# Kernel tuning notes

Measured on AMD Instinct MI355X. Metric: run time of the kernel, lower is better.

The kernel has to match this reference:

```python
import jax, jax.numpy as jnp
import numpy as np

GAMMA = 0.99
GAE_LAMBDA = 0.95
DONE_PROB = 0.01  # sparse episode terminations, typical for long-horizon trading envs


def setup_inputs() -> dict:
    key = jax.random.key(0)
    k1, k2, k3 = jax.random.split(key, 3)
    T, N = 2048, 4096  # rollout_len, num_envs
    rewards = jax.random.normal(k1, (T, N), dtype=jnp.float32)
    values = jax.random.normal(k2, (T, N), dtype=jnp.float32)
    dones = (jax.random.uniform(k3, (T, N)) < DONE_PROB).astype(jnp.float32)
    return {"rewards": rewards, "values": values, "dones": dones}


def reference(rewards, values, dones):
    # rewards/values/dones: [T, N]
    T, N = rewards.shape
    # bootstrap: beyond the last step, next_value = 0 and next_done = 1
    next_value = jnp.concatenate([values[1:], jnp.zeros((1, N), values.dtype)], axis=0)
    next_done = jnp.concatenate([dones[1:], jnp.ones((1, N), dones.dtype)], axis=0)
    nonterminal = 1.0 - next_done                      # [T, N]
    delta = rewards + GAMMA * next_value * nonterminal - values  # [T, N]

    def step(last_adv, xs):
        d, nt = xs                                     # each [N]
        adv = d + GAMMA * GAE_LAMBDA * nt * last_adv
        return adv, adv

    init = jnp.zeros((N,), rewards.dtype)
    _, advantages = jax.lax.scan(step, init, (delta, nonterminal), reverse=True)
    returns = advantages + values
    return advantages, returns
```

## Files before the change

### kernel.cpp

```cpp
#include <hip/hip_runtime.h>


#define T_LEN    2048
#define N_ENV    4096
#define NV4      (N_ENV / 4)
#define N_CHUNKS 128
#define CHUNK_L  (T_LEN / N_CHUNKS)

static constexpr float GAMMA = 0.99f;
static constexpr float GL    = 0.99f * 0.95f;

__global__ __launch_bounds__(256) void gae_phase1(
    const float4* __restrict__ rewards,
    const float4* __restrict__ values,
    const float4* __restrict__ dones,
    float4* __restrict__ Aout,
    float4* __restrict__ Pout)
{
    const int idx = blockIdx.x * blockDim.x + threadIdx.x;
    const int n4 = idx & (NV4 - 1);
    const int c  = idx >> 10;
    const int t_hi = c * CHUNK_L + (CHUNK_L - 1);

    float4 v_next, d_next;
    if (c == N_CHUNKS - 1) {
        v_next = make_float4(0.f, 0.f, 0.f, 0.f);
        d_next = make_float4(1.f, 1.f, 1.f, 1.f);
    } else {
        v_next = values[(t_hi + 1) * NV4 + n4];
        d_next = dones [(t_hi + 1) * NV4 + n4];
    }

    float4 A = make_float4(1.f, 1.f, 1.f, 1.f);
    float4 P = make_float4(0.f, 0.f, 0.f, 0.f);

    #pragma unroll
    for (int i = 0; i < CHUNK_L; ++i) {
        const int t = t_hi - i;
        const float4 r = rewards[t * NV4 + n4];
        const float4 v = values [t * NV4 + n4];
        const float4 d = dones  [t * NV4 + n4];
        #define STEP(X) { \
            const float nt    = 1.0f - d_next.X; \
            const float delta = fmaf(GAMMA * v_next.X, nt, r.X) - v.X; \
            const float cc    = GL * nt; \
            P.X = fmaf(cc, P.X, delta); \
            A.X = cc * A.X; \
            v_next.X = v.X; d_next.X = d.X; }
        STEP(x) STEP(y) STEP(z) STEP(w)
        #undef STEP
    }
    Aout[idx] = A;
    Pout[idx] = P;
}

__global__ __launch_bounds__(256) void gae_phase23(
    const float4* __restrict__ rewards,
    const float4* __restrict__ values,
    const float4* __restrict__ dones,
    const float4* __restrict__ Ain,
    const float4* __restrict__ Pin,
    float4* __restrict__ out)
{
    const int idx = blockIdx.x * blockDim.x + threadIdx.x;
    const int n4 = idx & (NV4 - 1);
    const int c  = idx >> 10;
    const int t_hi = c * CHUNK_L + (CHUNK_L - 1);

    float4 adv = make_float4(0.f, 0.f, 0.f, 0.f);
    #pragma unroll 4
    for (int c2 = N_CHUNKS - 1; c2 > c; --c2) {
        const float4 a = Ain[c2 * NV4 + n4];
        const float4 p = Pin[c2 * NV4 + n4];
        adv.x = fmaf(a.x, adv.x, p.x);
        adv.y = fmaf(a.y, adv.y, p.y);
        adv.z = fmaf(a.z, adv.z, p.z);
        adv.w = fmaf(a.w, adv.w, p.w);
    }

    float4 v_next, d_next;
    if (c == N_CHUNKS - 1) {
        v_next = make_float4(0.f, 0.f, 0.f, 0.f);
        d_next = make_float4(1.f, 1.f, 1.f, 1.f);
    } else {
        v_next = values[(t_hi + 1) * NV4 + n4];
        d_next = dones [(t_hi + 1) * NV4 + n4];
    }

    #pragma unroll
    for (int i = 0; i < CHUNK_L; ++i) {
        const int t = t_hi - i;
        const float4 r = rewards[t * NV4 + n4];
        const float4 v = values [t * NV4 + n4];
        const float4 d = dones  [t * NV4 + n4];
        float4 ret;
        #define STEP(X) { \
            const float nt    = 1.0f - d_next.X; \
            const float delta = fmaf(GAMMA * v_next.X, nt, r.X) - v.X; \
            const float cc    = GL * nt; \
            adv.X = fmaf(cc, adv.X, delta); \
            ret.X = adv.X + v.X; \
            v_next.X = v.X; d_next.X = d.X; }
        STEP(x) STEP(y) STEP(z) STEP(w)
        #undef STEP
        out[t * NV4 + n4]           = adv;
        out[(T_LEN + t) * NV4 + n4] = ret;
    }
}

extern "C" void kernel_launch(void* const* d_in, const int* in_sizes, int n_in,
                              void* d_out, int out_size, void* d_ws, size_t ws_size,
                              hipStream_t stream) {
    const float4* rewards = (const float4*)d_in[0];
    const float4* values  = (const float4*)d_in[1];
    const float4* dones   = (const float4*)d_in[2];
    float4* out = (float4*)d_out;

    float4* A = (float4*)d_ws;
    float4* P = A + (size_t)N_CHUNKS * NV4;

    const int blk = 256;
    gae_phase1<<<(N_CHUNKS * NV4) / blk, blk, 0, stream>>>(
        rewards, values, dones, A, P);
    gae_phase23<<<(N_CHUNKS * NV4) / blk, blk, 0, stream>>>(
        rewards, values, dones, A, P, out);
}
```

Measured before the change: 165.6 us.

## Fuse both GAE scan phases into one kernel with a grid-wide atomic barrier

Replaces the two-kernel chunked scan with one kernel. Each thread keeps its chunk's deltas, coefficients and values in registers across a global atomic-counter barrier, so rewards, values and dones are read from memory only once and the second launch goes away. This depends on all 512 blocks being resident at the same time, which launch bounds of 2 blocks per CU is meant to ensure. The cost is heavy register pressure and lower occupancy, and results could be wrong if the spin timeout ever fires before every block has arrived.

```diff
diff --git a/kernel.cpp b/kernel.cpp
--- a/kernel.cpp
+++ b/kernel.cpp
@@ -6,9 +6,101 @@
 #define NV4      (N_ENV / 4)
 #define N_CHUNKS 128
 #define CHUNK_L  (T_LEN / N_CHUNKS)
+#define NBLK     ((N_CHUNKS * NV4) / 256)
 
 static constexpr float GAMMA = 0.99f;
 static constexpr float GL    = 0.99f * 0.95f;
+
+__global__ __launch_bounds__(256, 2) void gae_fused(
+    const float4* __restrict__ rewards,
+    const float4* __restrict__ values,
+    const float4* __restrict__ dones,
+    float4* __restrict__ Abuf,
+    float4* __restrict__ Pbuf,
+    int*    __restrict__ counter,
+    float4* __restrict__ out)
+{
+    const int idx = blockIdx.x * blockDim.x + threadIdx.x;
+    const int n4 = idx & (NV4 - 1);
+    const int c  = idx >> 10;
+    const int t_hi = c * CHUNK_L + (CHUNK_L - 1);
+
+    float4 v_next, d_next;
+    if (c == N_CHUNKS - 1) {
+        v_next = make_float4(0.f, 0.f, 0.f, 0.f);
+        d_next = make_float4(1.f, 1.f, 1.f, 1.f);
+    } else {
+        v_next = values[(t_hi + 1) * NV4 + n4];
+        d_next = dones [(t_hi + 1) * NV4 + n4];
+    }
+
+    float4 dl[CHUNK_L], cc[CHUNK_L], vv[CHUNK_L];
+
+    float4 A = make_float4(1.f, 1.f, 1.f, 1.f);
+    float4 P = make_float4(0.f, 0.f, 0.f, 0.f);
+
+    #pragma unroll
+    for (int i = 0; i < CHUNK_L; ++i) {
+        const int t = t_hi - i;
+        const float4 r = rewards[t * NV4 + n4];
+        const float4 v = values [t * NV4 + n4];
+        const float4 d = dones  [t * NV4 + n4];
+        float4 dli, cci;
+        #define STEP(X) { \
+            const float nt    = 1.0f - d_next.X; \
+            const float delta = fmaf(GAMMA * v_next.X, nt, r.X) - v.X; \
+            const float co    = GL * nt; \
+            dli.X = delta; cci.X = co; \
+            P.X = fmaf(co, P.X, delta); \
+            A.X = co * A.X; \
+            v_next.X = v.X; d_next.X = d.X; }
+        STEP(x) STEP(y) STEP(z) STEP(w)
+        #undef STEP
+        dl[i] = dli; cc[i] = cci; vv[i] = v;
+    }
+    Abuf[idx] = A;
+    Pbuf[idx] = P;
+
+    __threadfence();
+    __syncthreads();
+    if (threadIdx.x == 0) {
+        __hip_atomic_fetch_add(counter, 1, __ATOMIC_ACQ_REL,
+                               __HIP_MEMORY_SCOPE_AGENT);
+        int spins = 0;
+        while (__hip_atomic_load(counter, __ATOMIC_RELAXED,
+                                 __HIP_MEMORY_SCOPE_AGENT) < NBLK &&
+               spins < (1 << 26)) {
+            __builtin_amdgcn_s_sleep(2);
+            ++spins;
+        }
+    }
+    __syncthreads();
+    __threadfence();
+
+    float4 adv = make_float4(0.f, 0.f, 0.f, 0.f);
+    #pragma unroll 4
+    for (int c2 = N_CHUNKS - 1; c2 > c; --c2) {
+        const float4 a = Abuf[c2 * NV4 + n4];
+        const float4 p = Pbuf[c2 * NV4 + n4];
+        adv.x = fmaf(a.x, adv.x, p.x);
+        adv.y = fmaf(a.y, adv.y, p.y);
+        adv.z = fmaf(a.z, adv.z, p.z);
+        adv.w = fmaf(a.w, adv.w, p.w);
+    }
+
+    #pragma unroll
+    for (int i = 0; i < CHUNK_L; ++i) {
+        const int t = t_hi - i;
+        float4 ret;
+        adv.x = fmaf(cc[i].x, adv.x, dl[i].x);  ret.x = adv.x + vv[i].x;
+        adv.y = fmaf(cc[i].y, adv.y, dl[i].y);  ret.y = adv.y + vv[i].y;
+        adv.z = fmaf(cc[i].z, adv.z, dl[i].z);  ret.z = adv.z + vv[i].z;
+        adv.w = fmaf(cc[i].w, adv.w, dl[i].w);  ret.w = adv.w + vv[i].w;
+        out[t * NV4 + n4]           = adv;
+        out[(T_LEN + t) * NV4 + n4] = ret;
+    }
+}
+
 
 __global__ __launch_bounds__(256) void gae_phase1(
     const float4* __restrict__ rewards,
@@ -43,9 +135,9 @@
         #define STEP(X) { \
             const float nt    = 1.0f - d_next.X; \
             const float delta = fmaf(GAMMA * v_next.X, nt, r.X) - v.X; \
-            const float cc    = GL * nt; \
-            P.X = fmaf(cc, P.X, delta); \
-            A.X = cc * A.X; \
+            const float co    = GL * nt; \
+            P.X = fmaf(co, P.X, delta); \
+            A.X = co * A.X; \
             v_next.X = v.X; d_next.X = d.X; }
         STEP(x) STEP(y) STEP(z) STEP(w)
         #undef STEP
@@ -97,8 +189,8 @@
         #define STEP(X) { \
             const float nt    = 1.0f - d_next.X; \
             const float delta = fmaf(GAMMA * v_next.X, nt, r.X) - v.X; \
-            const float cc    = GL * nt; \
-            adv.X = fmaf(cc, adv.X, delta); \
+            const float co    = GL * nt; \
+            adv.X = fmaf(co, adv.X, delta); \
             ret.X = adv.X + v.X; \
             v_next.X = v.X; d_next.X = d.X; }
         STEP(x) STEP(y) STEP(z) STEP(w)
@@ -118,10 +210,15 @@
 
     float4* A = (float4*)d_ws;
     float4* P = A + (size_t)N_CHUNKS * NV4;
-
-    const int blk = 256;
-    gae_phase1<<<(N_CHUNKS * NV4) / blk, blk, 0, stream>>>(
-        rewards, values, dones, A, P);
-    gae_phase23<<<(N_CHUNKS * NV4) / blk, blk, 0, stream>>>(
-        rewards, values, dones, A, P, out);
-}
+    const size_t apBytes = (size_t)2 * N_CHUNKS * NV4 * sizeof(float4);
+
+    if (ws_size >= apBytes + sizeof(int)) {
+        int* counter = (int*)((char*)d_ws + apBytes);
+        hipMemsetAsync(counter, 0, sizeof(int), stream);
+        gae_fused<<<NBLK, 256, 0, stream>>>(
+            rewards, values, dones, A, P, counter, out);
+    } else {
+        gae_phase1<<<NBLK, 256, 0, stream>>>(rewards, values, dones, A, P);
+        gae_phase23<<<NBLK, 256, 0, stream>>>(rewards, values, dones, A, P, out);
+    }
+}
```

Result: slower. 351.4 us (+112.2%).
